# Performance work log

Measured on AMD Instinct MI355X. Metric: run time of the kernel, lower is better.

Reference implementation:

```python
import jax, jax.numpy as jnp
import numpy as np

# dims
N, E, B, T = 1024, 8192, 4, 8          # nodes, edges, batch, time steps
IN, HID, H, NCLASS = 64, 64, 4, 7      # in_dim, nhidden, heads, nclass
K = N - NCLASS + 1                     # output-head conv width
NEG, EPS = 0.2, 1e-5


def setup_inputs() -> dict:
    key = jax.random.key(0)
    ks = jax.random.split(key, 24)
    p = lambda i, shape: jax.random.normal(ks[i], shape, jnp.float32) * 0.05
    inputs = jax.random.normal(ks[0], (B, IN, T, N), jnp.float32)
    src = jax.random.randint(ks[1], (E,), 0, N, jnp.int32)
    dst = jnp.repeat(jnp.arange(N, dtype=jnp.int32), E // N)  # every node has in-degree 8
    return {
        "inputs": inputs, "src": src, "dst": dst,
        "W0": p(2, (H * HID, IN)), "al0": p(3, (H, HID)), "ar0": p(4, (H, HID)),
        "W1": p(5, (H * HID, H * HID)), "al1": p(6, (H, HID)), "ar1": p(7, (H, HID)),
        "W2": p(8, (H * 1, H * HID)), "al2": p(9, (H, 1)), "ar2": p(10, (H, 1)),
        "Wres2": p(11, (H * 1, H * HID)),
        # Outputlayer
        "tc1_w": p(12, (H, H, T)), "tc1_b": p(13, (H,)),
        "ln1_g": jnp.ones((N, H), jnp.float32), "ln1_b": jnp.zeros((N, H), jnp.float32),
        "tc2_w": p(14, (1, H)), "tc2_b": p(15, (1,)),
        "ln2_g": jnp.ones((N, 1), jnp.float32), "ln2_b": jnp.zeros((N, 1), jnp.float32),
        "fc_w": p(16, (K,)), "fc_b": p(17, (1,)),
    }


def _gat_conv(h, src, dst, W, al, ar, res=None, act=None):
    # h: (N,B,T,F) -> feat: (N,B,T,H,D)
    heads, d = al.shape
    feat = (h @ W.T).reshape(N, B, T, heads, d)
    el = jnp.einsum('nbthd,hd->nbth', feat, al)
    er = jnp.einsum('nbthd,hd->nbth', feat, ar)
    e = jax.nn.leaky_relu(el[src] + er[dst], NEG)           # (E,B,T,H)
    emax = jax.ops.segment_max(e, dst, num_segments=N)
    ex = jnp.exp(e - emax[dst])
    den = jax.ops.segment_sum(ex, dst, num_segments=N)
    a = ex / den[dst]                                        # edge softmax over incoming edges
    out = jax.ops.segment_sum(feat[src] * a[..., None], dst, num_segments=N)  # (N,B,T,H,D)
    if res is not None:
        out = out + res
    if act is not None:
        out = act(out)
    return out


def reference(inputs, src, dst,
              W0, al0, ar0, W1, al1, ar1, W2, al2, ar2, Wres2,
              tc1_w, tc1_b, ln1_g, ln1_b, tc2_w, tc2_b, ln2_g, ln2_b, fc_w, fc_b):
    # (B,IN,T,N) -> (N,B,T,IN) : transpose(0,3).transpose(1,3)
    h = jnp.transpose(inputs.astype(jnp.float32), (3, 0, 2, 1))
    h1 = _gat_conv(h, src, dst, W0, al0, ar0, act=jax.nn.elu).reshape(N, B, T, H * HID)
    h2 = _gat_conv(h1, src, dst, W1, al1, ar1,
                   res=h1.reshape(N, B, T, H, HID), act=jax.nn.elu).reshape(N, B, T, H * HID)
    res2 = (h2 @ Wres2.T).reshape(N, B, T, H, 1)
    o = _gat_conv(h2, src, dst, W2, al2, ar2, res=res2)      # (N,B,T,H,1)
    # transpose(1,3).transpose(0,3).squeeze(-1) -> (B,H,T,N)
    x = jnp.transpose(o[..., 0], (1, 3, 2, 0))

    # Outputlayer
    # tconv1: Conv2d(H->H, kernel (T,1)) collapses time -> (B,H,N)
    x1 = jnp.einsum('oht,bhtn->bon', tc1_w, x) + tc1_b[None, :, None]
    # ln1: LayerNorm over (N,H) of (B,1,N,H)
    z = jnp.transpose(x1, (0, 2, 1))                          # (B,N,H)
    mu = z.mean(axis=(1, 2), keepdims=True)
    var = z.var(axis=(1, 2), keepdims=True)
    z = (z - mu) / jnp.sqrt(var + EPS) * ln1_g + ln1_b
    x1 = jnp.transpose(z, (0, 2, 1))                          # (B,H,N)
    # tconv2: 1x1 conv H->1 -> (B,1,N)
    x2 = jnp.einsum('oh,bhn->bon', tc2_w, x1) + tc2_b[None, :, None]
    # ln2: LayerNorm over (N,1)
    mu = x2.mean(axis=2, keepdims=True)
    var = x2.var(axis=2, keepdims=True)
    x2 = (x2 - mu) / jnp.sqrt(var + EPS) * ln2_g[:, 0] + ln2_b[:, 0]
    # fc: Conv2d(1->1, kernel (1,K)) sliding over nodes -> (B,NCLASS)
    xc = x2[:, :, None, :]                                    # (B,1,1,N) NCHW
    w = fc_w[None, None, None, :]                             # (1,1,1,K) OIHW
    out = jax.lax.conv_general_dilated(xc, w, (1, 1), 'VALID') + fc_b[None, :, None, None]
    return out[:, 0, 0, :]                                    # (B, NCLASS)
```

## Files before the change

kernel.cpp:

```cpp
#include <hip/hip_runtime.h>
#include <math.h>

#define NEGS 0.2f
#define EPSF 1e-5f

typedef short s16x8 __attribute__((ext_vector_type(8)));
typedef float f32x4 __attribute__((ext_vector_type(4)));

__device__ __forceinline__ float b2f(unsigned short u) {
  union { unsigned int i; float f; } v; v.i = ((unsigned int)u) << 16; return v.f;
}
__device__ __forceinline__ unsigned short f2b(float f) {
  union { float f; unsigned int i; } v; v.f = f;
  unsigned int x = v.i;
  return (unsigned short)((x + 0x7fffu + ((x >> 16) & 1u)) >> 16);
}

__device__ __forceinline__ float block_reduce1024(float v, float* red) {
  #pragma unroll
  for (int o = 32; o > 0; o >>= 1) v += __shfl_down(v, o);
  __syncthreads();
  if ((threadIdx.x & 63) == 0) red[threadIdx.x >> 6] = v;
  __syncthreads();
  float s = 0.f;
  #pragma unroll
  for (int i = 0; i < 16; ++i) s += red[i];
  return s;
}

__global__ __launch_bounds__(256) void k_feat0(
    const float* __restrict__ inp, const float* __restrict__ W0,
    const float* __restrict__ W1, const float* __restrict__ al,
    const float* __restrict__ ar, unsigned short* __restrict__ feat,
    float* __restrict__ el, float* __restrict__ er,
    unsigned short* __restrict__ W1b)
{
  const int tid = threadIdx.x;
  if (blockIdx.x >= 512) {
    const int j = (blockIdx.x - 512) * 256 + tid;
    float4 w4 = *(const float4*)&W1[j*4];
    ushort4 o4; o4.x=f2b(w4.x); o4.y=f2b(w4.y); o4.z=f2b(w4.z); o4.w=f2b(w4.w);
    *(ushort4*)&W1b[j*4] = o4;
    return;
  }
  __shared__ __align__(16) unsigned short Wl[256][72];
  __shared__ __align__(16) unsigned short At[64][72];
  const int bt = blockIdx.x & 31;
  const int n0 = (blockIdx.x >> 5) * 64;
  const int b  = bt >> 3, t = bt & 7;
  #pragma unroll
  for (int i = 0; i < 32; ++i) {
    int e = tid + i*256;
    float2 w2 = *(const float2*)&W0[e*2];
    unsigned int pk = ((unsigned int)f2b(w2.y) << 16) | (unsigned int)f2b(w2.x);
    *(unsigned int*)&At[0][0];
    *(unsigned int*)&Wl[(e*2) >> 6][(e*2) & 63] = pk;
  }
  {
    const int nn = tid & 63, cg = tid >> 6;
    #pragma unroll
    for (int c2 = 0; c2 < 8; ++c2) {
      int ch = (cg*8 + c2) * 2;
      float vx = inp[((size_t)(b*64 + ch  )*8 + t)*1024 + n0 + nn];
      float vy = inp[((size_t)(b*64 + ch+1)*8 + t)*1024 + n0 + nn];
      unsigned int pk = ((unsigned int)f2b(vy) << 16) | (unsigned int)f2b(vx);
      *(unsigned int*)&At[nn][ch] = pk;
    }
  }
  __syncthreads();
  const int w    = tid >> 6;
  const int lane = tid & 63;
  const int n16  = lane & 15;
  const int q    = lane >> 4;
  f32x4 acc[4][4];
  #pragma unroll
  for (int rt = 0; rt < 4; ++rt)
    #pragma unroll
    for (int ct = 0; ct < 4; ++ct) acc[rt][ct] = (f32x4){0.f,0.f,0.f,0.f};
  #pragma unroll
  for (int kc = 0; kc < 2; ++kc) {
    s16x8 af[4], bf[4];
    #pragma unroll
    for (int rt = 0; rt < 4; ++rt)
      af[rt] = *(const s16x8*)&At[rt*16 + n16][kc*32 + q*8];
    #pragma unroll
    for (int ct = 0; ct < 4; ++ct)
      bf[ct] = *(const s16x8*)&Wl[(w*4 + ct)*16 + n16][kc*32 + q*8];
    #pragma unroll
    for (int rt = 0; rt < 4; ++rt)
      #pragma unroll
      for (int ct = 0; ct < 4; ++ct)
        acc[rt][ct] = __builtin_amdgcn_mfma_f32_16x16x32_bf16(af[rt], bf[ct], acc[rt][ct], 0, 0, 0);
  }
  float alv[4], arv[4];
  #pragma unroll
  for (int ct = 0; ct < 4; ++ct) {
    alv[ct] = al[w*64 + ct*16 + n16];
    arv[ct] = ar[w*64 + ct*16 + n16];
  }
  #pragma unroll
  for (int rt = 0; rt < 4; ++rt) {
    #pragma unroll
    for (int reg = 0; reg < 4; ++reg) {
      float pl = acc[rt][0][reg]*alv[0] + acc[rt][1][reg]*alv[1]
               + acc[rt][2][reg]*alv[2] + acc[rt][3][reg]*alv[3];
      float pr = acc[rt][0][reg]*arv[0] + acc[rt][1][reg]*arv[1]
               + acc[rt][2][reg]*arv[2] + acc[rt][3][reg]*arv[3];
      #pragma unroll
      for (int o = 1; o < 16; o <<= 1) { pl += __shfl_xor(pl, o); pr += __shfl_xor(pr, o); }
      if (n16 == 0) {
        int r = (n0 + rt*16 + q*4 + reg)*32 + bt;
        el[r*4 + w] = pl;
        er[r*4 + w] = pr;
      }
    }
  }
  __syncthreads();
  unsigned short* Lb = &Wl[0][0];
  #pragma unroll
  for (int rt = 0; rt < 4; ++rt)
    #pragma unroll
    for (int ct = 0; ct < 4; ++ct)
      #pragma unroll
      for (int reg = 0; reg < 4; ++reg)
        Lb[(rt*16 + q*4 + reg)*256 + w*64 + ct*16 + n16] = f2b(acc[rt][ct][reg]);
  __syncthreads();
  #pragma unroll
  for (int i = 0; i < 8; ++i) {
    int u = tid + i*256;
    int m = u >> 5, off = (u & 31) * 8;
    *(s16x8*)&feat[(size_t)((n0 + m)*32 + bt)*256 + off] = *(const s16x8*)&Lb[m*256 + off];
  }
}

__global__ __launch_bounds__(256, 4) void k_agg0_feat1(
    const unsigned short* __restrict__ feat0, const float* __restrict__ el0,
    const float* __restrict__ er0, const int* __restrict__ src,
    const unsigned short* __restrict__ W1b, const float* __restrict__ al,
    const float* __restrict__ ar, unsigned short* __restrict__ h1b,
    unsigned short* __restrict__ feat1, float* __restrict__ el1, float* __restrict__ er1)
{
  __shared__ float wsm[8][32][4];
  __shared__ int   ssm[8];
  __shared__ __align__(16) unsigned short smbuf[32*264];
  unsigned short (*At)[264] = (unsigned short(*)[264])smbuf;
  unsigned short *Lb = smbuf;
  const int tid = threadIdx.x;
  const int n   = blockIdx.x;
  if (tid < 8) ssm[tid] = src[n*8 + tid];
  __syncthreads();
  if (tid < 128) {
    const int m = tid >> 2, h = tid & 3;
    const int rn = n*32 + m;
    const float erv = er0[rn*4 + h];
    float e[8]; float mx = -1e30f;
    #pragma unroll
    for (int j = 0; j < 8; ++j) {
      float v = el0[(ssm[j]*32 + m)*4 + h] + erv;
      v = v >= 0.f ? v : NEGS * v;
      e[j] = v; mx = fmaxf(mx, v);
    }
    float den = 0.f;
    #pragma unroll
    for (int j = 0; j < 8; ++j) { e[j] = __expf(e[j] - mx); den += e[j]; }
    const float inv = 1.f / den;
    #pragma unroll
    for (int j = 0; j < 8; ++j) wsm[j][m][h] = e[j] * inv;
  }
  __syncthreads();
  {
    const int hw2 = tid >> 5, l5 = tid & 31;
    const int c0 = l5 * 8, hh = l5 >> 3;
    #pragma unroll
    for (int p2 = 0; p2 < 2; ++p2) {
      const int mA = p2*16 + hw2, mB = mA + 8;
      s16x8 vA[8], vB[8];
      #pragma unroll
      for (int j = 0; j < 8; ++j) {
        vA[j] = *(const s16x8*)&feat0[(size_t)(ssm[j]*32 + mA)*256 + c0];
        vB[j] = *(const s16x8*)&feat0[(size_t)(ssm[j]*32 + mB)*256 + c0];
      }
      float aA[8] = {0,0,0,0,0,0,0,0}, aB[8] = {0,0,0,0,0,0,0,0};
      #pragma unroll
      for (int j = 0; j < 8; ++j) {
        const float wA = wsm[j][mA][hh], wB = wsm[j][mB][hh];
        #pragma unroll
        for (int i = 0; i < 8; ++i) {
          aA[i] = fmaf(wA, b2f((unsigned short)vA[j][i]), aA[i]);
          aB[i] = fmaf(wB, b2f((unsigned short)vB[j][i]), aB[i]);
        }
      }
      s16x8 oA, oB;
      #pragma unroll
      for (int i = 0; i < 8; ++i) {
        float xA = aA[i] > 0.f ? aA[i] : expm1f(aA[i]);
        float xB = aB[i] > 0.f ? aB[i] : expm1f(aB[i]);
        oA[i] = (short)f2b(xA); oB[i] = (short)f2b(xB);
      }
      *(s16x8*)&At[mA][c0] = oA;
      *(s16x8*)&At[mB][c0] = oB;
      *(s16x8*)&h1b[(size_t)(n*32 + mA)*256 + c0] = oA;
      *(s16x8*)&h1b[(size_t)(n*32 + mB)*256 + c0] = oB;
    }
  }
  __syncthreads();
  const int w    = tid >> 6;
  const int lane = tid & 63;
  const int n16  = lane & 15;
  const int q    = lane >> 4;
  const int r0   = n * 32;
  f32x4 acc[2][4];
  #pragma unroll
  for (int rt = 0; rt < 2; ++rt)
    #pragma unroll
    for (int ct = 0; ct < 4; ++ct) acc[rt][ct] = (f32x4){0.f,0.f,0.f,0.f};
  #pragma unroll
  for (int kc = 0; kc < 8; ++kc) {
    s16x8 af[2], bf[4];
    #pragma unroll
    for (int rt = 0; rt < 2; ++rt)
      af[rt] = *(const s16x8*)&At[rt*16 + n16][kc*32 + q*8];
    #pragma unroll
    for (int ct = 0; ct < 4; ++ct)
      bf[ct] = *(const s16x8*)&W1b[(size_t)((w*4 + ct)*16 + n16)*256 + kc*32 + q*8];
    #pragma unroll
    for (int rt = 0; rt < 2; ++rt)
      #pragma unroll
      for (int ct = 0; ct < 4; ++ct)
        acc[rt][ct] = __builtin_amdgcn_mfma_f32_16x16x32_bf16(af[rt], bf[ct], acc[rt][ct], 0, 0, 0);
  }
  float alv[4], arv[4];
  #pragma unroll
  for (int ct = 0; ct < 4; ++ct) {
    alv[ct] = al[w*64 + ct*16 + n16];
    arv[ct] = ar[w*64 + ct*16 + n16];
  }
  #pragma unroll
  for (int rt = 0; rt < 2; ++rt) {
    #pragma unroll
    for (int reg = 0; reg < 4; ++reg) {
      float pl = acc[rt][0][reg]*alv[0] + acc[rt][1][reg]*alv[1]
               + acc[rt][2][reg]*alv[2] + acc[rt][3][reg]*alv[3];
      float pr = acc[rt][0][reg]*arv[0] + acc[rt][1][reg]*arv[1]
               + acc[rt][2][reg]*arv[2] + acc[rt][3][reg]*arv[3];
      #pragma unroll
      for (int o = 1; o < 16; o <<= 1) { pl += __shfl_xor(pl, o); pr += __shfl_xor(pr, o); }
      if (n16 == 0) {
        int r = r0 + rt*16 + q*4 + reg;
        el1[r*4 + w] = pl;
        er1[r*4 + w] = pr;
      }
    }
  }
  __syncthreads();
  #pragma unroll
  for (int rt = 0; rt < 2; ++rt)
    #pragma unroll
    for (int ct = 0; ct < 4; ++ct)
      #pragma unroll
      for (int reg = 0; reg < 4; ++reg)
        Lb[(rt*16 + q*4 + reg)*256 + w*64 + ct*16 + n16] = f2b(acc[rt][ct][reg]);
  __syncthreads();
  #pragma unroll
  for (int i = 0; i < 4; ++i) {
    int u = tid + i*256;
    int row = u >> 5, off = (u & 31) * 8;
    *(s16x8*)&feat1[(size_t)(r0 + row)*256 + off] = *(const s16x8*)&Lb[row*256 + off];
  }
}

__global__ __launch_bounds__(256, 4) void k_agg1_proj(
    const unsigned short* __restrict__ feat1, const float* __restrict__ el,
    const float* __restrict__ er, const int* __restrict__ src,
    const unsigned short* __restrict__ h1b, const float* __restrict__ W2,
    const float* __restrict__ Wres2, float* __restrict__ feat2, float* __restrict__ res2)
{
  __shared__ float wsm[8][32][4];
  __shared__ int   ssm[8];
  __shared__ __align__(16) float Wp[8][256];
  const int tid = threadIdx.x;
  const int n   = blockIdx.x;
  if (tid < 8) ssm[tid] = src[n*8 + tid];
  for (int j2 = tid; j2 < 2048; j2 += 256) {
    int o = j2 >> 8, k = j2 & 255;
    Wp[o][k] = (o < 4) ? W2[o*256 + k] : Wres2[(o-4)*256 + k];
  }
  __syncthreads();
  if (tid < 128) {
    const int m = tid >> 2, h = tid & 3;
    const int rn = n*32 + m;
    const float erv = er[rn*4 + h];
    float e[8]; float mx = -1e30f;
    #pragma unroll
    for (int j = 0; j < 8; ++j) {
      float v = el[(ssm[j]*32 + m)*4 + h] + erv;
      v = v >= 0.f ? v : NEGS * v;
      e[j] = v; mx = fmaxf(mx, v);
    }
    float den = 0.f;
    #pragma unroll
    for (int j = 0; j < 8; ++j) { e[j] = __expf(e[j] - mx); den += e[j]; }
    const float inv = 1.f / den;
    #pragma unroll
    for (int j = 0; j < 8; ++j) wsm[j][m][h] = e[j] * inv;
  }
  __syncthreads();
  const int hw2 = tid >> 5, l5 = tid & 31;
  const int c0 = l5 * 8, hh = l5 >> 3;
  #pragma unroll
  for (int p2 = 0; p2 < 2; ++p2) {
    const int mA = p2*16 + hw2, mB = mA + 8;
    const int rnA = n*32 + mA, rnB = n*32 + mB;
    s16x8 vA[8], vB[8], rrA, rrB;
    rrA = *(const s16x8*)&h1b[(size_t)rnA*256 + c0];
    rrB = *(const s16x8*)&h1b[(size_t)rnB*256 + c0];
    #pragma unroll
    for (int j = 0; j < 8; ++j) {
      vA[j] = *(const s16x8*)&feat1[(size_t)(ssm[j]*32 + mA)*256 + c0];
      vB[j] = *(const s16x8*)&feat1[(size_t)(ssm[j]*32 + mB)*256 + c0];
    }
    float aA[8] = {0,0,0,0,0,0,0,0}, aB[8] = {0,0,0,0,0,0,0,0};
    #pragma unroll
    for (int j = 0; j < 8; ++j) {
      const float wA = wsm[j][mA][hh], wB = wsm[j][mB][hh];
      #pragma unroll
      for (int i = 0; i < 8; ++i) {
        aA[i] = fmaf(wA, b2f((unsigned short)vA[j][i]), aA[i]);
        aB[i] = fmaf(wB, b2f((unsigned short)vB[j][i]), aB[i]);
      }
    }
    #pragma unroll
    for (int i = 0; i < 8; ++i) {
      float xA = aA[i] + b2f((unsigned short)rrA[i]);
      float xB = aB[i] + b2f((unsigned short)rrB[i]);
      aA[i] = xA > 0.f ? xA : expm1f(xA);
      aB[i] = xB > 0.f ? xB : expm1f(xB);
    }
    #pragma unroll
    for (int o = 0; o < 8; ++o) {
      float4 wa = *(const float4*)&Wp[o][c0];
      float4 wb = *(const float4*)&Wp[o][c0 + 4];
      float pA = aA[0]*wa.x + aA[1]*wa.y + aA[2]*wa.z + aA[3]*wa.w
               + aA[4]*wb.x + aA[5]*wb.y + aA[6]*wb.z + aA[7]*wb.w;
      float pB = aB[0]*wa.x + aB[1]*wa.y + aB[2]*wa.z + aB[3]*wa.w
               + aB[4]*wb.x + aB[5]*wb.y + aB[6]*wb.z + aB[7]*wb.w;
      #pragma unroll
      for (int off = 1; off < 32; off <<= 1) {
        pA += __shfl_xor(pA, off);
        pB += __shfl_xor(pB, off);
      }
      if (l5 == 0) {
        if (o < 4) { feat2[rnA*4 + o] = pA; feat2[rnB*4 + o] = pB; }
        else       { res2[rnA*4 + (o-4)] = pA; res2[rnB*4 + (o-4)] = pB; }
      }
    }
  }
}

__global__ __launch_bounds__(128) void k_agg2(
    const float* __restrict__ feat2, const float* __restrict__ res2,
    const int* __restrict__ src, const float* __restrict__ al2,
    const float* __restrict__ ar2, const float* __restrict__ tc1w,
    const float* __restrict__ tc1b, float* __restrict__ x1)
{
  __shared__ float os[4][8][4];
  const int n = blockIdx.x;
  const int tid = threadIdx.x;
  const int b = tid >> 5, t = (tid >> 2) & 7, h = tid & 3;
  const int rn = n*32 + b*8 + t;
  const float av = al2[h], rv = ar2[h];
  const float erv = feat2[rn*4 + h] * rv;
  float f[8], e[8]; float m = -1e30f;
  #pragma unroll
  for (int j = 0; j < 8; ++j) {
    int s_ = src[n*8 + j];
    f[j] = feat2[(s_*32 + b*8 + t)*4 + h];
    float v = f[j]*av + erv;
    v = v >= 0.f ? v : NEGS * v;
    e[j] = v; m = fmaxf(m, v);
  }
  float den = 0.f, num = 0.f;
  #pragma unroll
  for (int j = 0; j < 8; ++j) { float ex = __expf(e[j]-m); den += ex; num = fmaf(ex, f[j], num); }
  os[b][t][h] = num/den + res2[rn*4 + h];
  __syncthreads();
  if (tid < 16) {
    int b2 = tid >> 2, o2 = tid & 3;
    float acc = tc1b[o2];
    #pragma unroll
    for (int hh = 0; hh < 4; ++hh)
      #pragma unroll
      for (int tt = 0; tt < 8; ++tt)
        acc = fmaf(tc1w[(o2*4 + hh)*8 + tt], os[b2][tt][hh], acc);
    x1[(b2*4 + o2)*1024 + n] = acc;
  }
}

__global__ __launch_bounds__(1024) void k_final(
    const float* __restrict__ x1, const float* __restrict__ ln1g,
    const float* __restrict__ ln1b, const float* __restrict__ tc2w,
    const float* __restrict__ tc2b, const float* __restrict__ ln2g,
    const float* __restrict__ ln2b, const float* __restrict__ fcw,
    const float* __restrict__ fcb, float* __restrict__ out)
{
  __shared__ float red[16];
  __shared__ float x2s[1024];
  const int b = blockIdx.x;
  const int tid = threadIdx.x;
  float s = 0.f, q = 0.f;
  for (int j = tid; j < 4096; j += 1024) {
    float v = x1[b*4096 + j];
    s += v; q += v*v;
  }
  float S = block_reduce1024(s, red);
  float Q = block_reduce1024(q, red);
  float mu  = S * (1.f/4096.f);
  float var = Q * (1.f/4096.f) - mu*mu;
  float inv = rsqrtf(var + EPSF);
  float tb = tc2b[0];
  const int nn = tid;
  float acc = tb;
  #pragma unroll
  for (int h = 0; h < 4; ++h) {
    float z = (x1[b*4096 + h*1024 + nn] - mu) * inv * ln1g[nn*4 + h] + ln1b[nn*4 + h];
    acc = fmaf(tc2w[h], z, acc);
  }
  float S2 = block_reduce1024(acc, red);
  float Q2 = block_reduce1024(acc*acc, red);
  float mu2  = S2 * (1.f/1024.f);
  float inv2 = rsqrtf(Q2 * (1.f/1024.f) - mu2*mu2 + EPSF);
  x2s[nn] = (acc - mu2) * inv2 * ln2g[nn] + ln2b[nn];
  __syncthreads();
  for (int c = 0; c < 7; ++c) {
    float p = (tid < 1018) ? x2s[c + tid] * fcw[tid] : 0.f;
    float P = block_reduce1024(p, red);
    if (tid == 0) out[b*7 + c] = P + fcb[0];
  }
}

extern "C" void kernel_launch(void* const* d_in, const int* in_sizes, int n_in,
                              void* d_out, int out_size, void* d_ws, size_t ws_size,
                              hipStream_t stream)
{
  const float* inp  = (const float*)d_in[0];
  const int*   src  = (const int*)  d_in[1];
  const float* W0   = (const float*)d_in[3];
  const float* al0  = (const float*)d_in[4];
  const float* ar0  = (const float*)d_in[5];
  const float* W1   = (const float*)d_in[6];
  const float* al1  = (const float*)d_in[7];
  const float* ar1  = (const float*)d_in[8];
  const float* W2   = (const float*)d_in[9];
  const float* al2  = (const float*)d_in[10];
  const float* ar2  = (const float*)d_in[11];
  const float* Wr2  = (const float*)d_in[12];
  const float* tc1w = (const float*)d_in[13];
  const float* tc1b = (const float*)d_in[14];
  const float* ln1g = (const float*)d_in[15];
  const float* ln1b = (const float*)d_in[16];
  const float* tc2w = (const float*)d_in[17];
  const float* tc2b = (const float*)d_in[18];
  const float* ln2g = (const float*)d_in[19];
  const float* ln2b = (const float*)d_in[20];
  const float* fcw  = (const float*)d_in[21];
  const float* fcb  = (const float*)d_in[22];
  float* out = (float*)d_out;

  unsigned short* W1b    = (unsigned short*)d_ws;
  unsigned short* featb0 = W1b    + 65536;
  unsigned short* featb1 = featb0 + 8388608;
  unsigned short* h1b    = featb1 + 8388608;
  float* el0   = (float*)(h1b + 8388608);
  float* er0   = el0   + 131072;
  float* el1   = er0   + 131072;
  float* er1   = el1   + 131072;
  float* feat2 = er1   + 131072;
  float* res2  = feat2 + 131072;
  float* x1    = res2  + 131072;

  k_feat0<<<dim3(576), dim3(256), 0, stream>>>(inp, W0, W1, al0, ar0,
                                               featb0, el0, er0, W1b);
  k_agg0_feat1<<<dim3(1024), dim3(256), 0, stream>>>(featb0, el0, er0, src, W1b, al1, ar1,
                                                     h1b, featb1, el1, er1);
  k_agg1_proj<<<dim3(1024), dim3(256), 0, stream>>>(featb1, el1, er1, src, h1b, W2, Wr2,
                                                    feat2, res2);
  k_agg2<<<dim3(1024), dim3(128), 0, stream>>>(feat2, res2, src, al2, ar2, tc1w, tc1b, x1);
  k_final<<<dim3(4), dim3(1024), 0, stream>>>(x1, ln1g, ln1b, tc2w, tc2b, ln2g, ln2b, fcw, fcb, out);
}
```

Before: 178.8 us.

## Split aggregation kernels into half-node blocks and load W0 fragments directly to registers

```diff
diff --git a/kernel.cpp b/kernel.cpp
--- a/kernel.cpp
+++ b/kernel.cpp
@@ -43,19 +43,28 @@
     *(ushort4*)&W1b[j*4] = o4;
     return;
   }
-  __shared__ __align__(16) unsigned short Wl[256][72];
   __shared__ __align__(16) unsigned short At[64][72];
+  __shared__ __align__(16) unsigned short Lb[64*256];
   const int bt = blockIdx.x & 31;
   const int n0 = (blockIdx.x >> 5) * 64;
   const int b  = bt >> 3, t = bt & 7;
-  #pragma unroll
-  for (int i = 0; i < 32; ++i) {
-    int e = tid + i*256;
-    float2 w2 = *(const float2*)&W0[e*2];
-    unsigned int pk = ((unsigned int)f2b(w2.y) << 16) | (unsigned int)f2b(w2.x);
-    *(unsigned int*)&At[0][0];
-    *(unsigned int*)&Wl[(e*2) >> 6][(e*2) & 63] = pk;
-  }
+  const int w    = tid >> 6;
+  const int lane = tid & 63;
+  const int n16  = lane & 15;
+  const int q    = lane >> 4;
+  s16x8 bf[2][4];
+  #pragma unroll
+  for (int kc = 0; kc < 2; ++kc)
+    #pragma unroll
+    for (int ct = 0; ct < 4; ++ct) {
+      const float* p = &W0[(size_t)((w*4 + ct)*16 + n16)*64 + kc*32 + q*8];
+      float4 wa = *(const float4*)p;
+      float4 wb = *(const float4*)(p + 4);
+      s16x8 o;
+      o[0]=(short)f2b(wa.x); o[1]=(short)f2b(wa.y); o[2]=(short)f2b(wa.z); o[3]=(short)f2b(wa.w);
+      o[4]=(short)f2b(wb.x); o[5]=(short)f2b(wb.y); o[6]=(short)f2b(wb.z); o[7]=(short)f2b(wb.w);
+      bf[kc][ct] = o;
+    }
   {
     const int nn = tid & 63, cg = tid >> 6;
     #pragma unroll
@@ -68,10 +77,6 @@
     }
   }
   __syncthreads();
-  const int w    = tid >> 6;
-  const int lane = tid & 63;
-  const int n16  = lane & 15;
-  const int q    = lane >> 4;
   f32x4 acc[4][4];
   #pragma unroll
   for (int rt = 0; rt < 4; ++rt)
@@ -79,18 +84,15 @@
     for (int ct = 0; ct < 4; ++ct) acc[rt][ct] = (f32x4){0.f,0.f,0.f,0.f};
   #pragma unroll
   for (int kc = 0; kc < 2; ++kc) {
-    s16x8 af[4], bf[4];
+    s16x8 af[4];
     #pragma unroll
     for (int rt = 0; rt < 4; ++rt)
       af[rt] = *(const s16x8*)&At[rt*16 + n16][kc*32 + q*8];
-    #pragma unroll
-    for (int ct = 0; ct < 4; ++ct)
-      bf[ct] = *(const s16x8*)&Wl[(w*4 + ct)*16 + n16][kc*32 + q*8];
     #pragma unroll
     for (int rt = 0; rt < 4; ++rt)
       #pragma unroll
       for (int ct = 0; ct < 4; ++ct)
-        acc[rt][ct] = __builtin_amdgcn_mfma_f32_16x16x32_bf16(af[rt], bf[ct], acc[rt][ct], 0, 0, 0);
+        acc[rt][ct] = __builtin_amdgcn_mfma_f32_16x16x32_bf16(af[rt], bf[kc][ct], acc[rt][ct], 0, 0, 0);
   }
   float alv[4], arv[4];
   #pragma unroll
@@ -115,8 +117,6 @@
       }
     }
   }
-  __syncthreads();
-  unsigned short* Lb = &Wl[0][0];
   #pragma unroll
   for (int rt = 0; rt < 4; ++rt)
     #pragma unroll
@@ -140,23 +140,24 @@
     const float* __restrict__ ar, unsigned short* __restrict__ h1b,
     unsigned short* __restrict__ feat1, float* __restrict__ el1, float* __restrict__ er1)
 {
-  __shared__ float wsm[8][32][4];
+  __shared__ float wsm[8][16][4];
   __shared__ int   ssm[8];
-  __shared__ __align__(16) unsigned short smbuf[32*264];
+  __shared__ __align__(16) unsigned short smbuf[16*264];
   unsigned short (*At)[264] = (unsigned short(*)[264])smbuf;
   unsigned short *Lb = smbuf;
   const int tid = threadIdx.x;
-  const int n   = blockIdx.x;
+  const int n   = blockIdx.x >> 1;
+  const int m0  = (blockIdx.x & 1) * 16;
   if (tid < 8) ssm[tid] = src[n*8 + tid];
   __syncthreads();
-  if (tid < 128) {
-    const int m = tid >> 2, h = tid & 3;
-    const int rn = n*32 + m;
+  if (tid < 64) {
+    const int ml = tid >> 2, h = tid & 3;
+    const int rn = n*32 + m0 + ml;
     const float erv = er0[rn*4 + h];
     float e[8]; float mx = -1e30f;
     #pragma unroll
     for (int j = 0; j < 8; ++j) {
-      float v = el0[(ssm[j]*32 + m)*4 + h] + erv;
+      float v = el0[(ssm[j]*32 + m0 + ml)*4 + h] + erv;
       v = v >= 0.f ? v : NEGS * v;
       e[j] = v; mx = fmaxf(mx, v);
     }
@@ -165,69 +166,59 @@
     for (int j = 0; j < 8; ++j) { e[j] = __expf(e[j] - mx); den += e[j]; }
     const float inv = 1.f / den;
     #pragma unroll
-    for (int j = 0; j < 8; ++j) wsm[j][m][h] = e[j] * inv;
+    for (int j = 0; j < 8; ++j) wsm[j][ml][h] = e[j] * inv;
   }
   __syncthreads();
   {
     const int hw2 = tid >> 5, l5 = tid & 31;
     const int c0 = l5 * 8, hh = l5 >> 3;
-    #pragma unroll
-    for (int p2 = 0; p2 < 2; ++p2) {
-      const int mA = p2*16 + hw2, mB = mA + 8;
-      s16x8 vA[8], vB[8];
-      #pragma unroll
-      for (int j = 0; j < 8; ++j) {
-        vA[j] = *(const s16x8*)&feat0[(size_t)(ssm[j]*32 + mA)*256 + c0];
-        vB[j] = *(const s16x8*)&feat0[(size_t)(ssm[j]*32 + mB)*256 + c0];
-      }
-      float aA[8] = {0,0,0,0,0,0,0,0}, aB[8] = {0,0,0,0,0,0,0,0};
-      #pragma unroll
-      for (int j = 0; j < 8; ++j) {
-        const float wA = wsm[j][mA][hh], wB = wsm[j][mB][hh];
-        #pragma unroll
-        for (int i = 0; i < 8; ++i) {
-          aA[i] = fmaf(wA, b2f((unsigned short)vA[j][i]), aA[i]);
-          aB[i] = fmaf(wB, b2f((unsigned short)vB[j][i]), aB[i]);
-        }
-      }
-      s16x8 oA, oB;
+    const int mA = m0 + hw2, mB = m0 + 8 + hw2;
+    s16x8 vA[8], vB[8];
+    #pragma unroll
+    for (int j = 0; j < 8; ++j) {
+      vA[j] = *(const s16x8*)&feat0[(size_t)(ssm[j]*32 + mA)*256 + c0];
+      vB[j] = *(const s16x8*)&feat0[(size_t)(ssm[j]*32 + mB)*256 + c0];
+    }
+    float aA[8] = {0,0,0,0,0,0,0,0}, aB[8] = {0,0,0,0,0,0,0,0};
+    #pragma unroll
+    for (int j = 0; j < 8; ++j) {
+      const float wA = wsm[j][hw2][hh], wB = wsm[j][8 + hw2][hh];
       #pragma unroll
       for (int i = 0; i < 8; ++i) {
-        float xA = aA[i] > 0.f ? aA[i] : expm1f(aA[i]);
-        float xB = aB[i] > 0.f ? aB[i] : expm1f(aB[i]);
-        oA[i] = (short)f2b(xA); oB[i] = (short)f2b(xB);
+        aA[i] = fmaf(wA, b2f((unsigned short)vA[j][i]), aA[i]);
+        aB[i] = fmaf(wB, b2f((unsigned short)vB[j][i]), aB[i]);
       }
-      *(s16x8*)&At[mA][c0] = oA;
-      *(s16x8*)&At[mB][c0] = oB;
-      *(s16x8*)&h1b[(size_t)(n*32 + mA)*256 + c0] = oA;
-      *(s16x8*)&h1b[(size_t)(n*32 + mB)*256 + c0] = oB;
-    }
+    }
+    s16x8 oA, oB;
+    #pragma unroll
+    for (int i = 0; i < 8; ++i) {
+      float xA = aA[i] > 0.f ? aA[i] : expm1f(aA[i]);
+      float xB = aB[i] > 0.f ? aB[i] : expm1f(aB[i]);
+      oA[i] = (short)f2b(xA); oB[i] = (short)f2b(xB);
+    }
+    *(s16x8*)&At[hw2][c0] = oA;
+    *(s16x8*)&At[8 + hw2][c0] = oB;
+    *(s16x8*)&h1b[(size_t)(n*32 + mA)*256 + c0] = oA;
+    *(s16x8*)&h1b[(size_t)(n*32 + mB)*256 + c0] = oB;
   }
   __syncthreads();
   const int w    = tid >> 6;
   const int lane = tid & 63;
   const int n16  = lane & 15;
   const int q    = lane >> 4;
-  const int r0   = n * 32;
-  f32x4 acc[2][4];
-  #pragma unroll
-  for (int rt = 0; rt < 2; ++rt)
-    #pragma unroll
-    for (int ct = 0; ct < 4; ++ct) acc[rt][ct] = (f32x4){0.f,0.f,0.f,0.f};
+  f32x4 acc[4];
+  #pragma unroll
+  for (int ct = 0; ct < 4; ++ct) acc[ct] = (f32x4){0.f,0.f,0.f,0.f};
   #pragma unroll
   for (int kc = 0; kc < 8; ++kc) {
-    s16x8 af[2], bf[4];
-    #pragma unroll
-    for (int rt = 0; rt < 2; ++rt)
-      af[rt] = *(const s16x8*)&At[rt*16 + n16][kc*32 + q*8];
+    s16x8 af = *(const s16x8*)&At[n16][kc*32 + q*8];
+    s16x8 bfr[4];
     #pragma unroll
     for (int ct = 0; ct < 4; ++ct)
-      bf[ct] = *(const s16x8*)&W1b[(size_t)((w*4 + ct)*16 + n16)*256 + kc*32 + q*8];
-    #pragma unroll
-    for (int rt = 0; rt < 2; ++rt)
-      #pragma unroll
-      for (int ct = 0; ct < 4; ++ct)
-        acc[rt][ct] = __builtin_amdgcn_mfma_f32_16x16x32_bf16(af[rt], bf[ct], acc[rt][ct], 0, 0, 0);
+      bfr[ct] = *(const s16x8*)&W1b[(size_t)((w*4 + ct)*16 + n16)*256 + kc*32 + q*8];
+    #pragma unroll
+    for (int ct = 0; ct < 4; ++ct)
+      acc[ct] = __builtin_amdgcn_mfma_f32_16x16x32_bf16(af, bfr[ct], acc[ct], 0, 0, 0);
   }
   float alv[4], arv[4];
   #pragma unroll
@@ -236,36 +227,31 @@
     arv[ct] = ar[w*64 + ct*16 + n16];
   }
   #pragma unroll
-  for (int rt = 0; rt < 2; ++rt) {
-    #pragma unroll
-    for (int reg = 0; reg < 4; ++reg) {
-      float pl = acc[rt][0][reg]*alv[0] + acc[rt][1][reg]*alv[1]
-               + acc[rt][2][reg]*alv[2] + acc[rt][3][reg]*alv[3];
-      float pr = acc[rt][0][reg]*arv[0] + acc[rt][1][reg]*arv[1]
-               + acc[rt][2][reg]*arv[2] + acc[rt][3][reg]*arv[3];
-      #pragma unroll
-      for (int o = 1; o < 16; o <<= 1) { pl += __shfl_xor(pl, o); pr += __shfl_xor(pr, o); }
-      if (n16 == 0) {
-        int r = r0 + rt*16 + q*4 + reg;
-        el1[r*4 + w] = pl;
-        er1[r*4 + w] = pr;
-      }
-    }
-  }
-  __syncthreads();
-  #pragma unroll
-  for (int rt = 0; rt < 2; ++rt)
-    #pragma unroll
-    for (int ct = 0; ct < 4; ++ct)
-      #pragma unroll
-      for (int reg = 0; reg < 4; ++reg)
-        Lb[(rt*16 + q*4 + reg)*256 + w*64 + ct*16 + n16] = f2b(acc[rt][ct][reg]);
-  __syncthreads();
-  #pragma unroll
-  for (int i = 0; i < 4; ++i) {
+  for (int reg = 0; reg < 4; ++reg) {
+    float pl = acc[0][reg]*alv[0] + acc[1][reg]*alv[1]
+             + acc[2][reg]*alv[2] + acc[3][reg]*alv[3];
+    float pr = acc[0][reg]*arv[0] + acc[1][reg]*arv[1]
+             + acc[2][reg]*arv[2] + acc[3][reg]*arv[3];
+    #pragma unroll
+    for (int o = 1; o < 16; o <<= 1) { pl += __shfl_xor(pl, o); pr += __shfl_xor(pr, o); }
+    if (n16 == 0) {
+      int r = n*32 + m0 + q*4 + reg;
+      el1[r*4 + w] = pl;
+      er1[r*4 + w] = pr;
+    }
+  }
+  __syncthreads();
+  #pragma unroll
+  for (int ct = 0; ct < 4; ++ct)
+    #pragma unroll
+    for (int reg = 0; reg < 4; ++reg)
+      Lb[(q*4 + reg)*256 + w*64 + ct*16 + n16] = f2b(acc[ct][reg]);
+  __syncthreads();
+  #pragma unroll
+  for (int i = 0; i < 2; ++i) {
     int u = tid + i*256;
     int row = u >> 5, off = (u & 31) * 8;
-    *(s16x8*)&feat1[(size_t)(r0 + row)*256 + off] = *(const s16x8*)&Lb[row*256 + off];
+    *(s16x8*)&feat1[(size_t)(n*32 + m0 + row)*256 + off] = *(const s16x8*)&Lb[row*256 + off];
   }
 }
 
@@ -275,25 +261,26 @@
     const unsigned short* __restrict__ h1b, const float* __restrict__ W2,
     const float* __restrict__ Wres2, float* __restrict__ feat2, float* __restrict__ res2)
 {
-  __shared__ float wsm[8][32][4];
+  __shared__ float wsm[8][16][4];
   __shared__ int   ssm[8];
   __shared__ __align__(16) float Wp[8][256];
   const int tid = threadIdx.x;
-  const int n   = blockIdx.x;
+  const int n   = blockIdx.x >> 1;
+  const int m0  = (blockIdx.x & 1) * 16;
   if (tid < 8) ssm[tid] = src[n*8 + tid];
   for (int j2 = tid; j2 < 2048; j2 += 256) {
     int o = j2 >> 8, k = j2 & 255;
     Wp[o][k] = (o < 4) ? W2[o*256 + k] : Wres2[(o-4)*256 + k];
   }
   __syncthreads();
-  if (tid < 128) {
-    const int m = tid >> 2, h = tid & 3;
-    const int rn = n*32 + m;
+  if (tid < 64) {
+    const int ml = tid >> 2, h = tid & 3;
+    const int rn = n*32 + m0 + ml;
     const float erv = er[rn*4 + h];
     float e[8]; float mx = -1e30f;
     #pragma unroll
     for (int j = 0; j < 8; ++j) {
-      float v = el[(ssm[j]*32 + m)*4 + h] + erv;
+      float v = el[(ssm[j]*32 + m0 + ml)*4 + h] + erv;
       v = v >= 0.f ? v : NEGS * v;
       e[j] = v; mx = fmaxf(mx, v);
     }
@@ -302,57 +289,54 @@
     for (int j = 0; j < 8; ++j) { e[j] = __expf(e[j] - mx); den += e[j]; }
     const float inv = 1.f / den;
     #pragma unroll
-    for (int j = 0; j < 8; ++j) wsm[j][m][h] = e[j] * inv;
+    for (int j = 0; j < 8; ++j) wsm[j][ml][h] = e[j] * inv;
   }
   __syncthreads();
   const int hw2 = tid >> 5, l5 = tid & 31;
   const int c0 = l5 * 8, hh = l5 >> 3;
-  #pragma unroll
-  for (int p2 = 0; p2 < 2; ++p2) {
-    const int mA = p2*16 + hw2, mB = mA + 8;
-    const int rnA = n*32 + mA, rnB = n*32 + mB;
-    s16x8 vA[8], vB[8], rrA, rrB;
-    rrA = *(const s16x8*)&h1b[(size_t)rnA*256 + c0];
-    rrB = *(const s16x8*)&h1b[(size_t)rnB*256 + c0];
-    #pragma unroll
-    for (int j = 0; j < 8; ++j) {
-      vA[j] = *(const s16x8*)&feat1[(size_t)(ssm[j]*32 + mA)*256 + c0];
-      vB[j] = *(const s16x8*)&feat1[(size_t)(ssm[j]*32 + mB)*256 + c0];
-    }
-    float aA[8] = {0,0,0,0,0,0,0,0}, aB[8] = {0,0,0,0,0,0,0,0};
-    #pragma unroll
-    for (int j = 0; j < 8; ++j) {
-      const float wA = wsm[j][mA][hh], wB = wsm[j][mB][hh];
-      #pragma unroll
-      for (int i = 0; i < 8; ++i) {
-        aA[i] = fmaf(wA, b2f((unsigned short)vA[j][i]), aA[i]);
-        aB[i] = fmaf(wB, b2f((unsigned short)vB[j][i]), aB[i]);
-      }
-    }
+  const int mA = m0 + hw2, mB = m0 + 8 + hw2;
+  const int rnA = n*32 + mA, rnB = n*32 + mB;
+  s16x8 vA[8], vB[8], rrA, rrB;
+  rrA = *(const s16x8*)&h1b[(size_t)rnA*256 + c0];
+  rrB = *(const s16x8*)&h1b[(size_t)rnB*256 + c0];
+  #pragma unroll
+  for (int j = 0; j < 8; ++j) {
+    vA[j] = *(const s16x8*)&feat1[(size_t)(ssm[j]*32 + mA)*256 + c0];
+    vB[j] = *(const s16x8*)&feat1[(size_t)(ssm[j]*32 + mB)*256 + c0];
+  }
+  float aA[8] = {0,0,0,0,0,0,0,0}, aB[8] = {0,0,0,0,0,0,0,0};
+  #pragma unroll
+  for (int j = 0; j < 8; ++j) {
+    const float wA = wsm[j][hw2][hh], wB = wsm[j][8 + hw2][hh];
     #pragma unroll
     for (int i = 0; i < 8; ++i) {
-      float xA = aA[i] + b2f((unsigned short)rrA[i]);
-      float xB = aB[i] + b2f((unsigned short)rrB[i]);
-      aA[i] = xA > 0.f ? xA : expm1f(xA);
-      aB[i] = xB > 0.f ? xB : expm1f(xB);
-    }
-    #pragma unroll
-    for (int o = 0; o < 8; ++o) {
-      float4 wa = *(const float4*)&Wp[o][c0];
-      float4 wb = *(const float4*)&Wp[o][c0 + 4];
-      float pA = aA[0]*wa.x + aA[1]*wa.y + aA[2]*wa.z + aA[3]*wa.w
-               + aA[4]*wb.x + aA[5]*wb.y + aA[6]*wb.z + aA[7]*wb.w;
-      float pB = aB[0]*wa.x + aB[1]*wa.y + aB[2]*wa.z + aB[3]*wa.w
-               + aB[4]*wb.x + aB[5]*wb.y + aB[6]*wb.z + aB[7]*wb.w;
-      #pragma unroll
-      for (int off = 1; off < 32; off <<= 1) {
-        pA += __shfl_xor(pA, off);
-        pB += __shfl_xor(pB, off);
-      }
-      if (l5 == 0) {
-        if (o < 4) { feat2[rnA*4 + o] = pA; feat2[rnB*4 + o] = pB; }
-        else       { res2[rnA*4 + (o-4)] = pA; res2[rnB*4 + (o-4)] = pB; }
-      }
+      aA[i] = fmaf(wA, b2f((unsigned short)vA[j][i]), aA[i]);
+      aB[i] = fmaf(wB, b2f((unsigned short)vB[j][i]), aB[i]);
+    }
+  }
+  #pragma unroll
+  for (int i = 0; i < 8; ++i) {
+    float xA = aA[i] + b2f((unsigned short)rrA[i]);
+    float xB = aB[i] + b2f((unsigned short)rrB[i]);
+    aA[i] = xA > 0.f ? xA : expm1f(xA);
+    aB[i] = xB > 0.f ? xB : expm1f(xB);
+  }
+  #pragma unroll
+  for (int o = 0; o < 8; ++o) {
+    float4 wa = *(const float4*)&Wp[o][c0];
+    float4 wb = *(const float4*)&Wp[o][c0 + 4];
+    float pA = aA[0]*wa.x + aA[1]*wa.y + aA[2]*wa.z + aA[3]*wa.w
+             + aA[4]*wb.x + aA[5]*wb.y + aA[6]*wb.z + aA[7]*wb.w;
+    float pB = aB[0]*wa.x + aB[1]*wa.y + aB[2]*wa.z + aB[3]*wa.w
+             + aB[4]*wb.x + aB[5]*wb.y + aB[6]*wb.z + aB[7]*wb.w;
+    #pragma unroll
+    for (int off = 1; off < 32; off <<= 1) {
+      pA += __shfl_xor(pA, off);
+      pB += __shfl_xor(pB, off);
+    }
+    if (l5 == 0) {
+      if (o < 4) { feat2[rnA*4 + o] = pA; feat2[rnB*4 + o] = pB; }
+      else       { res2[rnA*4 + (o-4)] = pA; res2[rnB*4 + (o-4)] = pB; }
     }
   }
 }
@@ -480,9 +464,9 @@
 
   k_feat0<<<dim3(576), dim3(256), 0, stream>>>(inp, W0, W1, al0, ar0,
                                                featb0, el0, er0, W1b);
-  k_agg0_feat1<<<dim3(1024), dim3(256), 0, stream>>>(featb0, el0, er0, src, W1b, al1, ar1,
+  k_agg0_feat1<<<dim3(2048), dim3(256), 0, stream>>>(featb0, el0, er0, src, W1b, al1, ar1,
                                                      h1b, featb1, el1, er1);
-  k_agg1_proj<<<dim3(1024), dim3(256), 0, stream>>>(featb1, el1, er1, src, h1b, W2, Wr2,
+  k_agg1_proj<<<dim3(2048), dim3(256), 0, stream>>>(featb1, el1, er1, src, h1b, W2, Wr2,
                                                     feat2, res2);
   k_agg2<<<dim3(1024), dim3(128), 0, stream>>>(feat2, res2, src, al2, ar2, tc1w, tc1b, x1);
   k_final<<<dim3(4), dim3(1024), 0, stream>>>(x1, ln1g, ln1b, tc2w, tc2b, ln2g, ln2b, fcw, fcb, out);
```

New measurement: 197.1 us. 1.1x slower.
